# Optimization experiments

Hardware: AMD Instinct MI355X
Metric: run time of the kernel (lower is better)

## Reference

```python
import jax, jax.numpy as jnp
import numpy as np

P, K, L = 2048, 10, 3        # pairs, paths-per-pair (cap 10), max path length
E, H = 256, 512              # kg_embed_dim, node_dim
N_ENT, N_REL = 10000, 200
N_HEADS = 4


def setup_inputs() -> dict:
    key = jax.random.key(0)
    ks = jax.random.split(key, 20)
    s = 0.05  # weight scale for numerical stability
    return {
        'rel_idx': jax.random.randint(ks[0], (P, K, L), 0, N_REL, dtype=jnp.int32),
        'ent_idx': jax.random.randint(ks[1], (P, K, L), 0, N_ENT, dtype=jnp.int32),
        'path_lens': jax.random.randint(ks[2], (P, K), 0, L + 1, dtype=jnp.int32),
        'rel_table': jax.random.normal(ks[3], (N_REL, E), jnp.float32),
        'ent_table': jax.random.normal(ks[4], (N_ENT, E), jnp.float32),
        'kg_proj_w': jax.random.normal(ks[5], (H, E), jnp.float32) * s,
        'kg_proj_b': jax.random.normal(ks[6], (H,), jnp.float32) * s,
        'w_ih': jax.random.normal(ks[7], (4 * H, 2 * H), jnp.float32) * s,
        'w_hh': jax.random.normal(ks[8], (4 * H, H), jnp.float32) * s,
        'b_ih': jax.random.normal(ks[9], (4 * H,), jnp.float32) * s,
        'b_hh': jax.random.normal(ks[10], (4 * H,), jnp.float32) * s,
        'attn_in_w': jax.random.normal(ks[11], (3 * H, H), jnp.float32) * s,
        'attn_in_b': jax.random.normal(ks[12], (3 * H,), jnp.float32) * s,
        'attn_out_w': jax.random.normal(ks[13], (H, H), jnp.float32) * s,
        'attn_out_b': jax.random.normal(ks[14], (H,), jnp.float32) * s,
        'path_proj_w': jax.random.normal(ks[15], (H, H), jnp.float32) * s,
        'path_proj_b': jax.random.normal(ks[16], (H,), jnp.float32) * s,
    }


def _forward(rel_idx, ent_idx, path_lens, rel_table, ent_table, kg_proj_w, kg_proj_b,
             w_ih, w_hh, b_ih, b_hh, attn_in_w, attn_in_b, attn_out_w, attn_out_b,
             path_proj_w, path_proj_b):
    # --- encode_path, batched over all P*K paths ---
    rel_e = rel_table[rel_idx]                      # [P,K,L,E]
    ent_e = ent_table[ent_idx]                      # [P,K,L,E]
    rel_p = rel_e @ kg_proj_w.T + kg_proj_b         # [P,K,L,H]
    ent_p = ent_e @ kg_proj_w.T + kg_proj_b
    x = jnp.concatenate([rel_p, ent_p], axis=-1)    # [P,K,L,2H]
    Npk = P * K
    xs = x.reshape(Npk, L, 2 * H).transpose(1, 0, 2)  # [L,N,2H]

    h0 = jnp.zeros((Npk, H), x.dtype)
    c0 = jnp.zeros((Npk, H), x.dtype)

    def lstm_step(carry, x_t):
        h, c = carry
        g = x_t @ w_ih.T + b_ih + h @ w_hh.T + b_hh   # [N,4H], torch gate order i,f,g,o
        i, f, gg, o = jnp.split(g, 4, axis=-1)
        c = jax.nn.sigmoid(f) * c + jax.nn.sigmoid(i) * jnp.tanh(gg)
        h = jax.nn.sigmoid(o) * jnp.tanh(c)
        return (h, c), h

    _, hs = jax.lax.scan(lstm_step, (h0, c0), xs)     # [L,N,H]
    hs = hs.transpose(1, 0, 2)                        # [N,L,H]
    lens = path_lens.reshape(Npk)                     # [N]
    last = jnp.clip(lens - 1, 0, L - 1)
    h_last = jnp.take_along_axis(hs, last[:, None, None], axis=1)[:, 0]  # [N,H]
    path_emb = jnp.where(lens[:, None] > 0, h_last, 0.0).reshape(P, K, H)

    # --- per-pair multi-head self-attention over K path embeddings ---
    wq, wk, wv = jnp.split(attn_in_w, 3, axis=0)
    bq, bk, bv = jnp.split(attn_in_b, 3, axis=0)
    Dh = H // N_HEADS
    q = (path_emb @ wq.T + bq).reshape(P, K, N_HEADS, Dh)
    k = (path_emb @ wk.T + bk).reshape(P, K, N_HEADS, Dh)
    v = (path_emb @ wv.T + bv).reshape(P, K, N_HEADS, Dh)
    scores = jnp.einsum('pqhd,pkhd->phqk', q, k) / jnp.sqrt(jnp.array(Dh, x.dtype))
    attn = jax.nn.softmax(scores, axis=-1)
    ctx = jnp.einsum('phqk,pkhd->pqhd', attn, v).reshape(P, K, H)
    attn_out = ctx @ attn_out_w.T + attn_out_b        # [P,K,H]
    agg = attn_out.mean(axis=1)                       # [P,H]  (aggregated.mean(dim=1))
    return agg @ path_proj_w.T + path_proj_b          # [P,H]


def reference(rel_idx, ent_idx, path_lens, rel_table, ent_table, kg_proj_w, kg_proj_b,
              w_ih, w_hh, b_ih, b_hh, attn_in_w, attn_in_b, attn_out_w, attn_out_b,
              path_proj_w, path_proj_b):
    return _forward(rel_idx, ent_idx, path_lens, rel_table, ent_table, kg_proj_w,
                    kg_proj_b, w_ih, w_hh, b_ih, b_hh, attn_in_w, attn_in_b,
                    attn_out_w, attn_out_b, path_proj_w, path_proj_b)
```

## Files before the change

### kernel.cpp

```cpp
#include <hip/hip_runtime.h>
#include <cstdint>
#include <cstddef>

#define PP 2048
#define KK 10
#define HH 512
#define NPK (PP*KK)
#define ENT_PAD 10112
#define REL_PAD 256
#define HALF_PAIRS 1024
#define HALF_ROWS (HALF_PAIRS*KK)

using f32x4  = __attribute__((ext_vector_type(4))) float;
using short8 = __attribute__((ext_vector_type(8))) short;

__device__ __forceinline__ float sigf(float x) { return 1.0f / (1.0f + expf(-x)); }

__device__ __forceinline__ ushort f2bf(float x) {
    union { float f; uint32_t u; } v; v.f = x;
    uint32_t r = v.u + 0x7FFF + ((v.u >> 16) & 1);
    return (ushort)(r >> 16);
}
__device__ __forceinline__ float bf2f(ushort u) {
    union { uint32_t u; float f; } v; v.u = ((uint32_t)u) << 16;
    return v.f;
}

__global__ __launch_bounds__(256) void perm_bias(int* __restrict__ perm,
                                                 float* __restrict__ bihh,
                                                 const float* __restrict__ b_ih,
                                                 const float* __restrict__ b_hh) {
    int p = blockIdx.x * 256 + threadIdx.x;
    if (p < 2048) {
        int uh = p >> 6, g = (p >> 4) & 3, ul = p & 15;
        int old = g * 512 + uh * 16 + ul;
        perm[p] = old;
        bihh[p] = b_ih[old] + b_hh[old];
    }
}

__global__ __launch_bounds__(256) void transpose_k(const float* __restrict__ src,
                                                   float* __restrict__ dst, int R, int C) {
    __shared__ float t[32][33];
    int bx = blockIdx.x * 32, by = blockIdx.y * 32;
    int x = threadIdx.x & 31, y = threadIdx.x >> 5;
    for (int i = y; i < 32; i += 8) {
        int r = by + i, c = bx + x;
        if (r < R && c < C) t[i][x] = src[(size_t)r * C + c];
    }
    __syncthreads();
    for (int i = y; i < 32; i += 8) {
        int c = bx + i, r = by + x;
        if (r < R && c < C) dst[(size_t)c * R + r] = t[x][i];
    }
}

__global__ __launch_bounds__(256) void rowdot(const float* __restrict__ A, int lda,
                                              const float* __restrict__ vec, int Kd,
                                              const float* __restrict__ add1,
                                              float* __restrict__ out, int M) {
    int w = threadIdx.x >> 6, lane = threadIdx.x & 63;
    int row = blockIdx.x * 4 + w;
    if (row >= M) return;
    float acc = 0.f;
    for (int k = lane; k < Kd; k += 64) acc += A[(size_t)row * lda + k] * vec[k];
    for (int off = 32; off; off >>= 1) acc += __shfl_down(acc, off, 64);
    if (lane == 0) {
        float r = acc;
        if (add1) r += add1[row];
        out[row] = r;
    }
}

__global__ __launch_bounds__(256) void f2bf_split2d(const float* __restrict__ src,
                                                    int lda, int col0,
                                                    ushort* __restrict__ hi,
                                                    ushort* __restrict__ lo,
                                                    int nsrc_rows, int ncols, int ndst_rows,
                                                    const int* __restrict__ perm) {
    int i = blockIdx.x * 256 + threadIdx.x;
    int nc4 = ncols >> 2;
    if (i >= ndst_rows * nc4) return;
    int row = i / nc4, c4 = i % nc4;
    ushort4 h = make_ushort4(0, 0, 0, 0), l = make_ushort4(0, 0, 0, 0);
    if (row < nsrc_rows) {
        int sr = perm ? perm[row] : row;
        float4 v = *reinterpret_cast<const float4*>(src + (size_t)sr * lda + col0 + c4 * 4);
        h = make_ushort4(f2bf(v.x), f2bf(v.y), f2bf(v.z), f2bf(v.w));
        l = make_ushort4(f2bf(v.x - bf2f(h.x)), f2bf(v.y - bf2f(h.y)),
                         f2bf(v.z - bf2f(h.z)), f2bf(v.w - bf2f(h.w)));
    }
    reinterpret_cast<ushort4*>(hi)[i] = h;
    reinterpret_cast<ushort4*>(lo)[i] = l;
}

__global__ __launch_bounds__(256) void f2bf_k(const float* __restrict__ s,
                                              ushort* __restrict__ d, int n4) {
    int i = blockIdx.x * 256 + threadIdx.x;
    if (i < n4) {
        float4 v = reinterpret_cast<const float4*>(s)[i];
        reinterpret_cast<ushort4*>(d)[i] = make_ushort4(f2bf(v.x), f2bf(v.y), f2bf(v.z), f2bf(v.w));
    }
}

__global__ __launch_bounds__(256) void f2bf_perm_rows(const float* __restrict__ s,
                                                      ushort* __restrict__ d,
                                                      const int* __restrict__ perm,
                                                      int nrows, int ncols4) {
    int i = blockIdx.x * 256 + threadIdx.x;
    if (i >= nrows * ncols4) return;
    int row = i / ncols4, c4 = i % ncols4;
    int sr = perm[row];
    float4 v = reinterpret_cast<const float4*>(s + (size_t)sr * ncols4 * 4)[c4];
    reinterpret_cast<ushort4*>(d + (size_t)row * ncols4 * 4)[c4] =
        make_ushort4(f2bf(v.x), f2bf(v.y), f2bf(v.z), f2bf(v.w));
}

__global__ __launch_bounds__(256) void gemm_bf16(
    const ushort* __restrict__ A, const ushort* __restrict__ B,
    float* __restrict__ C, int M, int N, int K, int ldc,
    const float* __restrict__ bias)
{
    __shared__ ushort As[128 * 64];
    __shared__ ushort Bs[128 * 64];
    int tid = threadIdx.x;
    int lane = tid & 63;
    int w = tid >> 6;
    int wr = w >> 1, wc = w & 1;
    int col0 = blockIdx.x * 128, row0 = blockIdx.y * 128;

    f32x4 acc[4][4];
#pragma unroll
    for (int m = 0; m < 4; ++m)
#pragma unroll
        for (int n = 0; n < 4; ++n) acc[m][n] = {0.f, 0.f, 0.f, 0.f};

    int rA = lane & 15;
    int kq = lane >> 4;

    for (int kt = 0; kt < K; kt += 64) {
#pragma unroll
        for (int it = 0; it < 4; ++it) {
            int c = it * 256 + tid;
            int row = c >> 3, ch = c & 7;
            int cs = ch ^ (row & 7);
            uint4 va = *reinterpret_cast<const uint4*>(A + (size_t)(row0 + row) * K + kt + ch * 8);
            *reinterpret_cast<uint4*>(&As[(size_t)row * 64 + cs * 8]) = va;
            uint4 vb = *reinterpret_cast<const uint4*>(B + (size_t)(col0 + row) * K + kt + ch * 8);
            *reinterpret_cast<uint4*>(&Bs[(size_t)row * 64 + cs * 8]) = vb;
        }
        __syncthreads();
#pragma unroll
        for (int s = 0; s < 2; ++s) {
            int csw = (s * 4 + kq) ^ (rA & 7);
            short8 af[4], bfr[4];
#pragma unroll
            for (int m = 0; m < 4; ++m) {
                int rowA = wr * 64 + m * 16 + rA;
                af[m] = *reinterpret_cast<const short8*>(&As[(size_t)rowA * 64 + csw * 8]);
            }
#pragma unroll
            for (int n = 0; n < 4; ++n) {
                int rowB = wc * 64 + n * 16 + rA;
                bfr[n] = *reinterpret_cast<const short8*>(&Bs[(size_t)rowB * 64 + csw * 8]);
            }
#pragma unroll
            for (int m = 0; m < 4; ++m)
#pragma unroll
                for (int n = 0; n < 4; ++n)
                    acc[m][n] = __builtin_amdgcn_mfma_f32_16x16x32_bf16(af[m], bfr[n], acc[m][n], 0, 0, 0);
        }
        __syncthreads();
    }
#pragma unroll
    for (int n = 0; n < 4; ++n) {
        int gcol = col0 + wc * 64 + n * 16 + rA;
        float bv = bias ? bias[gcol] : 0.f;
#pragma unroll
        for (int m = 0; m < 4; ++m) {
            int grow0 = row0 + wr * 64 + m * 16 + kq * 4;
#pragma unroll
            for (int r = 0; r < 4; ++r)
                C[(size_t)(grow0 + r) * ldc + gcol] = acc[m][n][r] + bv;
        }
    }
}

__global__ __launch_bounds__(256) void gemm_bf16s(
    const ushort* __restrict__ Ah, const ushort* __restrict__ Al,
    const ushort* __restrict__ Bh, const ushort* __restrict__ Bl,
    float* __restrict__ C, int M, int N, int K, int ldc,
    const float* __restrict__ bias)
{
    __shared__ ushort Ash[128 * 64];
    __shared__ ushort Asl[128 * 64];
    __shared__ ushort Bsh[128 * 64];
    __shared__ ushort Bsl[128 * 64];
    int tid = threadIdx.x;
    int lane = tid & 63;
    int w = tid >> 6;
    int wr = w >> 1, wc = w & 1;
    int col0 = blockIdx.x * 128, row0 = blockIdx.y * 128;

    f32x4 acc[4][4];
#pragma unroll
    for (int m = 0; m < 4; ++m)
#pragma unroll
        for (int n = 0; n < 4; ++n) acc[m][n] = {0.f, 0.f, 0.f, 0.f};

    int rA = lane & 15;
    int kq = lane >> 4;

    for (int kt = 0; kt < K; kt += 64) {
#pragma unroll
        for (int it = 0; it < 4; ++it) {
            int c = it * 256 + tid;
            int row = c >> 3, ch = c & 7;
            int cs = ch ^ (row & 7);
            size_t ga = (size_t)(row0 + row) * K + kt + ch * 8;
            size_t gb = (size_t)(col0 + row) * K + kt + ch * 8;
            size_t la = (size_t)row * 64 + cs * 8;
            *reinterpret_cast<uint4*>(&Ash[la]) = *reinterpret_cast<const uint4*>(Ah + ga);
            *reinterpret_cast<uint4*>(&Asl[la]) = *reinterpret_cast<const uint4*>(Al + ga);
            *reinterpret_cast<uint4*>(&Bsh[la]) = *reinterpret_cast<const uint4*>(Bh + gb);
            *reinterpret_cast<uint4*>(&Bsl[la]) = *reinterpret_cast<const uint4*>(Bl + gb);
        }
        __syncthreads();
#pragma unroll
        for (int s = 0; s < 2; ++s) {
            int csw = (s * 4 + kq) ^ (rA & 7);
            short8 xh[4], yh[4], t4[4];
#pragma unroll
            for (int m = 0; m < 4; ++m) {
                int rowA = wr * 64 + m * 16 + rA;
                xh[m] = *reinterpret_cast<const short8*>(&Ash[(size_t)rowA * 64 + csw * 8]);
            }
#pragma unroll
            for (int n = 0; n < 4; ++n) {
                int rowB = wc * 64 + n * 16 + rA;
                yh[n] = *reinterpret_cast<const short8*>(&Bsh[(size_t)rowB * 64 + csw * 8]);
            }
#pragma unroll
            for (int m = 0; m < 4; ++m)
#pragma unroll
                for (int n = 0; n < 4; ++n)
                    acc[m][n] = __builtin_amdgcn_mfma_f32_16x16x32_bf16(xh[m], yh[n], acc[m][n], 0, 0, 0);
#pragma unroll
            for (int n = 0; n < 4; ++n) {
                int rowB = wc * 64 + n * 16 + rA;
                t4[n] = *reinterpret_cast<const short8*>(&Bsl[(size_t)rowB * 64 + csw * 8]);
            }
#pragma unroll
            for (int m = 0; m < 4; ++m)
#pragma unroll
                for (int n = 0; n < 4; ++n)
                    acc[m][n] = __builtin_amdgcn_mfma_f32_16x16x32_bf16(xh[m], t4[n], acc[m][n], 0, 0, 0);
#pragma unroll
            for (int m = 0; m < 4; ++m) {
                int rowA = wr * 64 + m * 16 + rA;
                t4[m] = *reinterpret_cast<const short8*>(&Asl[(size_t)rowA * 64 + csw * 8]);
            }
#pragma unroll
            for (int m = 0; m < 4; ++m)
#pragma unroll
                for (int n = 0; n < 4; ++n)
                    acc[m][n] = __builtin_amdgcn_mfma_f32_16x16x32_bf16(t4[m], yh[n], acc[m][n], 0, 0, 0);
        }
        __syncthreads();
    }
#pragma unroll
    for (int n = 0; n < 4; ++n) {
        int gcol = col0 + wc * 64 + n * 16 + rA;
        float bv = bias ? bias[gcol] : 0.f;
#pragma unroll
        for (int m = 0; m < 4; ++m) {
            int grow0 = row0 + wr * 64 + m * 16 + kq * 4;
#pragma unroll
            for (int r = 0; r < 4; ++r)
                C[(size_t)(grow0 + r) * ldc + gcol] = acc[m][n][r] + bv;
        }
    }
}

__global__ __launch_bounds__(256) void gemm_lstm(
    const ushort* __restrict__ A, const ushort* __restrict__ B,
    const float* __restrict__ relg, const float* __restrict__ entg,
    const int* __restrict__ rel_idx, const int* __restrict__ ent_idx,
    const int* __restrict__ lens_,
    ushort* __restrict__ hbuf, float* __restrict__ cbuf, ushort* __restrict__ pemb,
    int t)
{
    __shared__ ushort As[128 * 64];
    __shared__ ushort Bs[128 * 64];
    const int K = 512;
    int tid = threadIdx.x;
    int lane = tid & 63;
    int w = tid >> 6;
    int wr = w >> 1, wc = w & 1;
    int col0 = blockIdx.x * 128, row0 = blockIdx.y * 128;

    f32x4 acc[4][4];
#pragma unroll
    for (int m = 0; m < 4; ++m)
#pragma unroll
        for (int n = 0; n < 4; ++n) acc[m][n] = {0.f, 0.f, 0.f, 0.f};

    int rA = lane & 15;
    int kq = lane >> 4;

    for (int kt = 0; kt < K; kt += 64) {
#pragma unroll
        for (int it = 0; it < 4; ++it) {
            int c = it * 256 + tid;
            int row = c >> 3, ch = c & 7;
            int cs = ch ^ (row & 7);
            uint4 va = *reinterpret_cast<const uint4*>(A + (size_t)(row0 + row) * K + kt + ch * 8);
            *reinterpret_cast<uint4*>(&As[(size_t)row * 64 + cs * 8]) = va;
            uint4 vb = *reinterpret_cast<const uint4*>(B + (size_t)(col0 + row) * K + kt + ch * 8);
            *reinterpret_cast<uint4*>(&Bs[(size_t)row * 64 + cs * 8]) = vb;
        }
        __syncthreads();
#pragma unroll
        for (int s = 0; s < 2; ++s) {
            int csw = (s * 4 + kq) ^ (rA & 7);
            short8 af[4], bfr[4];
#pragma unroll
            for (int m = 0; m < 4; ++m) {
                int rowA = wr * 64 + m * 16 + rA;
                af[m] = *reinterpret_cast<const short8*>(&As[(size_t)rowA * 64 + csw * 8]);
            }
#pragma unroll
            for (int n = 0; n < 4; ++n) {
                int rowB = wc * 64 + n * 16 + rA;
                bfr[n] = *reinterpret_cast<const short8*>(&Bs[(size_t)rowB * 64 + csw * 8]);
            }
#pragma unroll
            for (int m = 0; m < 4; ++m)
#pragma unroll
                for (int n = 0; n < 4; ++n)
                    acc[m][n] = __builtin_amdgcn_mfma_f32_16x16x32_bf16(af[m], bfr[n], acc[m][n], 0, 0, 0);
        }
        __syncthreads();
    }

    int uh = blockIdx.x * 2 + wc;
    int u  = uh * 16 + rA;
    int colbase = uh * 64 + rA;
#pragma unroll
    for (int m = 0; m < 4; ++m) {
#pragma unroll
        for (int r = 0; r < 4; ++r) {
            int n = row0 + wr * 64 + m * 16 + kq * 4 + r;
            int ri = rel_idx[n * 3 + t];
            int ei = ent_idx[n * 3 + t];
            const float* rr = relg + (size_t)ri * 2048 + colbase;
            const float* er = entg + (size_t)ei * 2048 + colbase;
            float gi = acc[m][0][r] + rr[0]  + er[0];
            float gf = acc[m][1][r] + rr[16] + er[16];
            float gg = acc[m][2][r] + rr[32] + er[32];
            float go = acc[m][3][r] + rr[48] + er[48];
            float cold = cbuf[(size_t)n * 512 + u];
            float cn = sigf(gf) * cold + sigf(gi) * tanhf(gg);
            float hn = sigf(go) * tanhf(cn);
            cbuf[(size_t)n * 512 + u] = cn;
            ushort hu = f2bf(hn);
            hbuf[(size_t)n * 512 + u] = hu;
            int len = lens_[n];
            int last = len - 1;
            if (last < 0) last = 0;
            if (last > 2) last = 2;
            if (last == t) pemb[(size_t)n * 512 + u] = (len > 0) ? hu : (ushort)0;
        }
    }
}

__global__ __launch_bounds__(256) void lstm_t0(
    const float* __restrict__ relg, const float* __restrict__ entg,
    const int* __restrict__ rel_idx, const int* __restrict__ ent_idx,
    const int* __restrict__ lens_,
    ushort* __restrict__ hbuf, float* __restrict__ cbuf, ushort* __restrict__ pemb,
    int nrows)
{
    int gid = blockIdx.x * 256 + threadIdx.x;
    if (gid >= nrows * 128) return;
    int nl = gid >> 7, q = gid & 127;
    int uh = q >> 2, ul4 = q & 3;
    int ri = rel_idx[nl * 3];
    int ei = ent_idx[nl * 3];
    const float4* rg = reinterpret_cast<const float4*>(relg + (size_t)ri * 2048);
    const float4* eg = reinterpret_cast<const float4*>(entg + (size_t)ei * 2048);
    int b4 = uh * 16 + ul4;
    float4 gi = rg[b4], gf = rg[b4 + 4], gg = rg[b4 + 8], go = rg[b4 + 12];
    float4 e0 = eg[b4], e1 = eg[b4 + 4], e2 = eg[b4 + 8], e3 = eg[b4 + 12];
    gi.x += e0.x; gi.y += e0.y; gi.z += e0.z; gi.w += e0.w;
    gf.x += e1.x; gf.y += e1.y; gf.z += e1.z; gf.w += e1.w;
    gg.x += e2.x; gg.y += e2.y; gg.z += e2.z; gg.w += e2.w;
    go.x += e3.x; go.y += e3.y; go.z += e3.z; go.w += e3.w;
    (void)gf;
    float4 cn, hn;
    cn.x = sigf(gi.x) * tanhf(gg.x); hn.x = sigf(go.x) * tanhf(cn.x);
    cn.y = sigf(gi.y) * tanhf(gg.y); hn.y = sigf(go.y) * tanhf(cn.y);
    cn.z = sigf(gi.z) * tanhf(gg.z); hn.z = sigf(go.z) * tanhf(cn.z);
    cn.w = sigf(gi.w) * tanhf(gg.w); hn.w = sigf(go.w) * tanhf(cn.w);
    int u4 = uh * 4 + ul4;
    reinterpret_cast<float4*>(cbuf + (size_t)nl * 512)[u4] = cn;
    ushort4 hu = make_ushort4(f2bf(hn.x), f2bf(hn.y), f2bf(hn.z), f2bf(hn.w));
    reinterpret_cast<ushort4*>(hbuf + (size_t)nl * 512)[u4] = hu;
    int len = lens_[nl];
    int last = len - 1;
    if (last < 0) last = 0;
    if (last > 2) last = 2;
    if (last == 0) {
        ushort4 pv = (len > 0) ? hu : make_ushort4(0, 0, 0, 0);
        reinterpret_cast<ushort4*>(pemb + (size_t)nl * 512)[u4] = pv;
    }
}

__global__ __launch_bounds__(256) void attn_kernel(const float* __restrict__ qkv,
                                                   float* __restrict__ mctx, int pair0)
{
    __shared__ float qk[10][1024];
    __shared__ float sc[4][10][10];
    __shared__ float wb[4][10];
    int tid = threadIdx.x;
    const float* base = qkv + (size_t)blockIdx.x * 10 * 1536;
    for (int i = tid; i < 2560; i += 256) {
        int row = i >> 8, c4 = i & 255;
        reinterpret_cast<float4*>(&qk[row][0])[c4] =
            reinterpret_cast<const float4*>(base + (size_t)row * 1536)[c4];
    }
    __syncthreads();
    const float scale = 0.08838834764831845f;
    for (int idx = tid; idx < 400; idx += 256) {
        int h = idx / 100, rem = idx % 100, qi = rem / 10, ki = rem % 10;
        const float* qp = &qk[qi][h * 128];
        const float* kp = &qk[ki][512 + h * 128];
        float a = 0.f;
        for (int d = 0; d < 128; ++d) a += qp[d] * kp[d];
        sc[h][qi][ki] = a * scale;
    }
    __syncthreads();
    if (tid < 40) {
        int h = tid / 10, qi = tid % 10;
        float m = -1e30f;
        for (int ki = 0; ki < 10; ++ki) m = fmaxf(m, sc[h][qi][ki]);
        float ex[10]; float s = 0.f;
        for (int ki = 0; ki < 10; ++ki) { ex[ki] = expf(sc[h][qi][ki] - m); s += ex[ki]; }
        float inv = 1.f / s;
        for (int ki = 0; ki < 10; ++ki) sc[h][qi][ki] = ex[ki] * inv;
    }
    __syncthreads();
    if (tid < 40) {
        int h = tid / 10, ki = tid % 10;
        float s = 0.f;
        for (int qi = 0; qi < 10; ++qi) s += sc[h][qi][ki];
        wb[h][ki] = s * 0.1f;
    }
    __syncthreads();
    for (int e = tid; e < 512; e += 256) {
        int h = e >> 7, d = e & 127;
        float a = 0.f;
        for (int ki = 0; ki < 10; ++ki)
            a += wb[h][ki] * base[(size_t)ki * 1536 + 1024 + h * 128 + d];
        mctx[(size_t)(pair0 + blockIdx.x) * 512 + e] = a;
    }
}

extern "C" void kernel_launch(void* const* d_in, const int* in_sizes, int n_in,
                              void* d_out, int out_size, void* d_ws, size_t ws_size,
                              hipStream_t stream)
{
    const int* rel_idx     = (const int*)d_in[0];
    const int* ent_idx     = (const int*)d_in[1];
    const int* path_lens   = (const int*)d_in[2];
    const float* rel_table = (const float*)d_in[3];
    const float* ent_table = (const float*)d_in[4];
    const float* kg_proj_w = (const float*)d_in[5];
    const float* kg_proj_b = (const float*)d_in[6];
    const float* w_ih      = (const float*)d_in[7];
    const float* w_hh      = (const float*)d_in[8];
    const float* b_ih      = (const float*)d_in[9];
    const float* b_hh      = (const float*)d_in[10];
    const float* attn_in_w = (const float*)d_in[11];
    const float* attn_in_b = (const float*)d_in[12];
    const float* attn_out_w = (const float*)d_in[13];
    const float* attn_out_b = (const float*)d_in[14];
    const float* path_proj_w = (const float*)d_in[15];
    const float* path_proj_b = (const float*)d_in[16];
    float* out = (float*)d_out;
    (void)in_sizes; (void)n_in; (void)out_size; (void)ws_size;

    float* ws = (float*)d_ws;
    size_t off = 0;
    auto alloc = [&](size_t n) { float* p = ws + off; off += (n + 63) & ~(size_t)63; return p; };
    int*    perm  = (int*)alloc(2048);
    float*  bihh  = alloc(2048);
    float*  bcomb = alloc(512);
    float*  relg  = alloc((size_t)REL_PAD * 2048);
    float*  entg  = alloc((size_t)ENT_PAD * 2048);
    float*  mctx  = alloc((size_t)PP * 512);
    ushort* whhB  = (ushort*)alloc((size_t)2048 * 256);
    ushort* aiwB  = (ushort*)alloc((size_t)1536 * 256);
    ushort* pch   = (ushort*)alloc((size_t)NPK * 256);
    ushort* Wch   = (ushort*)alloc((size_t)512 * 256);
    ushort* Wcl   = (ushort*)alloc((size_t)512 * 256);
    float* R = alloc((size_t)21000000);

    size_t ro = 0;
    auto ral = [&](size_t n) { float* p = R + ro; ro += n; return p; };
    ushort* kgWh  = (ushort*)ral(65536);   ushort* kgWl  = (ushort*)ral(65536);
    ushort* relBh = (ushort*)ral(32768);   ushort* relBl = (ushort*)ral(32768);
    ushort* entBh = (ushort*)ral(1294336); ushort* entBl = (ushort*)ral(1294336);
    ushort* wrelh = (ushort*)ral(524288);  ushort* wrell = (ushort*)ral(524288);
    ushort* wenth = (ushort*)ral(524288);  ushort* wentl = (ushort*)ral(524288);
    float*  rel_pf = ral(131072);
    float*  ent_pf = ral(5177344);
    ushort* rel_ph = (ushort*)ral(65536);   ushort* rel_pl = (ushort*)ral(65536);
    ushort* ent_ph = (ushort*)ral(2588672); ushort* ent_pl = (ushort*)ral(2588672);
    float*  aoT    = ral(262144);
    ushort* pph  = (ushort*)ral(131072); ushort* ppl  = (ushort*)ral(131072);
    ushort* aoTh = (ushort*)ral(131072); ushort* aoTl = (ushort*)ral(131072);
    float*  WcombF = ral(262144);
    float*  cb = R;
    ushort* hA = (ushort*)(R + 10485760);
    ushort* hB = (ushort*)(R + 15728640);
    float*  qkv = R;
    ushort* mch = (ushort*)R;
    ushort* mcl = (ushort*)(R + 524288);

    auto split = [&](const float* src, int lda, int col0, ushort* hi, ushort* lo,
                     int nsrc, int ncols, int ndst, const int* pm) {
        int total = ndst * (ncols / 4);
        f2bf_split2d<<<(total + 255) / 256, 256, 0, stream>>>(src, lda, col0, hi, lo, nsrc, ncols, ndst, pm);
    };
    auto gemms = [&](const ushort* Ah, const ushort* Al, const ushort* Bh, const ushort* Bl,
                     float* Cp, int M, int N, int Kd, int ldc, const float* bias) {
        gemm_bf16s<<<dim3((unsigned)(N / 128), (unsigned)(M / 128)), 256, 0, stream>>>(
            Ah, Al, Bh, Bl, Cp, M, N, Kd, ldc, bias);
    };

    perm_bias<<<8, 256, 0, stream>>>(perm, bihh, b_ih, b_hh);
    transpose_k<<<dim3(16, 16), 256, 0, stream>>>(attn_out_w, aoT, 512, 512);
    split(kg_proj_w, 256, 0, kgWh, kgWl, 512, 256, 512, nullptr);
    split(rel_table, 256, 0, relBh, relBl, 200, 256, REL_PAD, nullptr);
    split(ent_table, 256, 0, entBh, entBl, 10000, 256, ENT_PAD, nullptr);
    split(w_ih, 1024, 0,   wrelh, wrell, 2048, 512, 2048, perm);
    split(w_ih, 1024, 512, wenth, wentl, 2048, 512, 2048, perm);
    split(path_proj_w, 512, 0, pph, ppl, 512, 512, 512, nullptr);
    split(aoT, 512, 0, aoTh, aoTl, 512, 512, 512, nullptr);
    f2bf_perm_rows<<<1024, 256, 0, stream>>>(w_hh, whhB, perm, 2048, 128);
    f2bf_k<<<768, 256, 0, stream>>>(attn_in_w, aiwB, 1536 * 128);
    rowdot<<<128, 256, 0, stream>>>(path_proj_w, 512, attn_out_b, 512, path_proj_b, bcomb, 512);

    gemms(relBh, relBl, kgWh, kgWl, rel_pf, REL_PAD, 512, 256, 512, kg_proj_b);
    gemms(entBh, entBl, kgWh, kgWl, ent_pf, ENT_PAD, 512, 256, 512, kg_proj_b);
    split(rel_pf, 512, 0, rel_ph, rel_pl, REL_PAD, 512, REL_PAD, nullptr);
    split(ent_pf, 512, 0, ent_ph, ent_pl, ENT_PAD, 512, ENT_PAD, nullptr);
    gemms(rel_ph, rel_pl, wrelh, wrell, relg, REL_PAD, 2048, 512, 2048, bihh);
    gemms(ent_ph, ent_pl, wenth, wentl, entg, ENT_PAD, 2048, 512, 2048, nullptr);
    gemms(pph, ppl, aoTh, aoTl, WcombF, 512, 512, 512, 512, nullptr);
    split(WcombF, 512, 0, Wch, Wcl, 512, 512, 512, nullptr);

    lstm_t0<<<(NPK * 128) / 256, 256, 0, stream>>>(
        relg, entg, rel_idx, ent_idx, path_lens, hA, cb, pch, NPK);
    gemm_lstm<<<dim3(16, 160), 256, 0, stream>>>(
        hA, whhB, relg, entg, rel_idx, ent_idx, path_lens, hB, cb, pch, 1);
    gemm_lstm<<<dim3(16, 160), 256, 0, stream>>>(
        hB, whhB, relg, entg, rel_idx, ent_idx, path_lens, hA, cb, pch, 2);

    for (int h = 0; h < 2; ++h) {
        gemm_bf16<<<dim3(12, 80), 256, 0, stream>>>(
            pch + (size_t)h * HALF_ROWS * 512, aiwB, qkv, HALF_ROWS, 1536, 512, 1536, attn_in_b);
        attn_kernel<<<HALF_PAIRS, 256, 0, stream>>>(qkv, mctx, h * HALF_PAIRS);
    }

    split(mctx, 512, 0, mch, mcl, 2048, 512, 2048, nullptr);
    gemms(mch, mcl, Wch, Wcl, out, 2048, 512, 512, 512, bcomb);
}
```

Baseline: 745.2 us.

## Fuse bf16 hi/lo splits into GEMM epilogues and interleave gate columns

The split-GEMM epilogue can now write bf16 hi/lo pairs directly, so the separate split kernels after the kg projection, the Wcomb GEMM and the attention output are removed, along with their fp32 intermediates. Gate columns of the input-gate tables are reordered so that the four gates of each unit sit next to each other, letting the LSTM kernels fetch them with one float4 load per table instead of four strided scalar loads. gemm_lstm also remaps its flattened block index with a swizzle to change L2 locality across tiles. The cost is an extra permutation array and a more complex epilogue.

```diff
diff --git a/kernel.cpp b/kernel.cpp
--- a/kernel.cpp
+++ b/kernel.cpp
@@ -26,16 +26,19 @@
     return v.f;
 }
 
-__global__ __launch_bounds__(256) void perm_bias(int* __restrict__ perm,
-                                                 float* __restrict__ bihh,
-                                                 const float* __restrict__ b_ih,
-                                                 const float* __restrict__ b_hh) {
-    int p = blockIdx.x * 256 + threadIdx.x;
-    if (p < 2048) {
-        int uh = p >> 6, g = (p >> 4) & 3, ul = p & 15;
-        int old = g * 512 + uh * 16 + ul;
-        perm[p] = old;
-        bihh[p] = b_ih[old] + b_hh[old];
+__global__ __launch_bounds__(256) void perm_bias2(int* __restrict__ perm_p,
+                                                  int* __restrict__ perm_q,
+                                                  float* __restrict__ bihh_q,
+                                                  const float* __restrict__ b_ih,
+                                                  const float* __restrict__ b_hh) {
+    int i = blockIdx.x * 256 + threadIdx.x;
+    if (i < 2048) {
+        int uh = i >> 6, g = (i >> 4) & 3, ul = i & 15;
+        perm_p[i] = g * 512 + uh * 16 + ul;
+        int u = i >> 2, gq = i & 3;
+        int oldq = gq * 512 + u;
+        perm_q[i] = oldq;
+        bihh_q[i] = b_ih[oldq] + b_hh[oldq];
     }
 }
 
@@ -189,7 +192,8 @@
 __global__ __launch_bounds__(256) void gemm_bf16s(
     const ushort* __restrict__ Ah, const ushort* __restrict__ Al,
     const ushort* __restrict__ Bh, const ushort* __restrict__ Bl,
-    float* __restrict__ C, int M, int N, int K, int ldc,
+    float* __restrict__ C, ushort* __restrict__ Chi, ushort* __restrict__ Clo,
+    int M, int N, int K, int ldc,
     const float* __restrict__ bias)
 {
     __shared__ ushort Ash[128 * 64];
@@ -276,8 +280,16 @@
         for (int m = 0; m < 4; ++m) {
             int grow0 = row0 + wr * 64 + m * 16 + kq * 4;
 #pragma unroll
-            for (int r = 0; r < 4; ++r)
-                C[(size_t)(grow0 + r) * ldc + gcol] = acc[m][n][r] + bv;
+            for (int r = 0; r < 4; ++r) {
+                float v = acc[m][n][r] + bv;
+                size_t idx = (size_t)(grow0 + r) * ldc + gcol;
+                if (C) C[idx] = v;
+                if (Chi) {
+                    ushort h = f2bf(v);
+                    Chi[idx] = h;
+                    Clo[idx] = f2bf(v - bf2f(h));
+                }
+            }
         }
     }
 }
@@ -293,11 +305,14 @@
     __shared__ ushort As[128 * 64];
     __shared__ ushort Bs[128 * 64];
     const int K = 512;
+    int L = blockIdx.x;
+    int swz = (L & 7) * 320 + (L >> 3);
+    int bx = swz & 15, by = swz >> 4;
     int tid = threadIdx.x;
     int lane = tid & 63;
     int w = tid >> 6;
     int wr = w >> 1, wc = w & 1;
-    int col0 = blockIdx.x * 128, row0 = blockIdx.y * 128;
+    int col0 = bx * 128, row0 = by * 128;
 
     f32x4 acc[4][4];
 #pragma unroll
@@ -343,9 +358,10 @@
         __syncthreads();
     }
 
-    int uh = blockIdx.x * 2 + wc;
+    int uh = bx * 2 + wc;
     int u  = uh * 16 + rA;
-    int colbase = uh * 64 + rA;
+    const float4* rel4 = reinterpret_cast<const float4*>(relg);
+    const float4* ent4 = reinterpret_cast<const float4*>(entg);
 #pragma unroll
     for (int m = 0; m < 4; ++m) {
 #pragma unroll
@@ -353,12 +369,12 @@
             int n = row0 + wr * 64 + m * 16 + kq * 4 + r;
             int ri = rel_idx[n * 3 + t];
             int ei = ent_idx[n * 3 + t];
-            const float* rr = relg + (size_t)ri * 2048 + colbase;
-            const float* er = entg + (size_t)ei * 2048 + colbase;
-            float gi = acc[m][0][r] + rr[0]  + er[0];
-            float gf = acc[m][1][r] + rr[16] + er[16];
-            float gg = acc[m][2][r] + rr[32] + er[32];
-            float go = acc[m][3][r] + rr[48] + er[48];
+            float4 rv = rel4[(size_t)ri * 512 + u];
+            float4 ev = ent4[(size_t)ei * 512 + u];
+            float gi = acc[m][0][r] + rv.x + ev.x;
+            float gf = acc[m][1][r] + rv.y + ev.y;
+            float gg = acc[m][2][r] + rv.z + ev.z;
+            float go = acc[m][3][r] + rv.w + ev.w;
             float cold = cbuf[(size_t)n * 512 + u];
             float cn = sigf(gf) * cold + sigf(gi) * tanhf(gg);
             float hn = sigf(go) * tanhf(cn);
@@ -384,40 +400,37 @@
     int gid = blockIdx.x * 256 + threadIdx.x;
     if (gid >= nrows * 128) return;
     int nl = gid >> 7, q = gid & 127;
-    int uh = q >> 2, ul4 = q & 3;
     int ri = rel_idx[nl * 3];
     int ei = ent_idx[nl * 3];
-    const float4* rg = reinterpret_cast<const float4*>(relg + (size_t)ri * 2048);
-    const float4* eg = reinterpret_cast<const float4*>(entg + (size_t)ei * 2048);
-    int b4 = uh * 16 + ul4;
-    float4 gi = rg[b4], gf = rg[b4 + 4], gg = rg[b4 + 8], go = rg[b4 + 12];
-    float4 e0 = eg[b4], e1 = eg[b4 + 4], e2 = eg[b4 + 8], e3 = eg[b4 + 12];
-    gi.x += e0.x; gi.y += e0.y; gi.z += e0.z; gi.w += e0.w;
-    gf.x += e1.x; gf.y += e1.y; gf.z += e1.z; gf.w += e1.w;
-    gg.x += e2.x; gg.y += e2.y; gg.z += e2.z; gg.w += e2.w;
-    go.x += e3.x; go.y += e3.y; go.z += e3.z; go.w += e3.w;
-    (void)gf;
+    const float4* rg = reinterpret_cast<const float4*>(relg) + (size_t)ri * 512;
+    const float4* eg = reinterpret_cast<const float4*>(entg) + (size_t)ei * 512;
     float4 cn, hn;
-    cn.x = sigf(gi.x) * tanhf(gg.x); hn.x = sigf(go.x) * tanhf(cn.x);
-    cn.y = sigf(gi.y) * tanhf(gg.y); hn.y = sigf(go.y) * tanhf(cn.y);
-    cn.z = sigf(gi.z) * tanhf(gg.z); hn.z = sigf(go.z) * tanhf(cn.z);
-    cn.w = sigf(gi.w) * tanhf(gg.w); hn.w = sigf(go.w) * tanhf(cn.w);
-    int u4 = uh * 4 + ul4;
-    reinterpret_cast<float4*>(cbuf + (size_t)nl * 512)[u4] = cn;
+#pragma unroll
+    for (int j = 0; j < 4; ++j) {
+        float4 a = rg[q * 4 + j];
+        float4 b = eg[q * 4 + j];
+        float gi = a.x + b.x, gg = a.z + b.z, go = a.w + b.w;
+        float c = sigf(gi) * tanhf(gg);
+        float h = sigf(go) * tanhf(c);
+        (&cn.x)[j] = c;
+        (&hn.x)[j] = h;
+    }
+    reinterpret_cast<float4*>(cbuf + (size_t)nl * 512)[q] = cn;
     ushort4 hu = make_ushort4(f2bf(hn.x), f2bf(hn.y), f2bf(hn.z), f2bf(hn.w));
-    reinterpret_cast<ushort4*>(hbuf + (size_t)nl * 512)[u4] = hu;
+    reinterpret_cast<ushort4*>(hbuf + (size_t)nl * 512)[q] = hu;
     int len = lens_[nl];
     int last = len - 1;
     if (last < 0) last = 0;
     if (last > 2) last = 2;
     if (last == 0) {
         ushort4 pv = (len > 0) ? hu : make_ushort4(0, 0, 0, 0);
-        reinterpret_cast<ushort4*>(pemb + (size_t)nl * 512)[u4] = pv;
+        reinterpret_cast<ushort4*>(pemb + (size_t)nl * 512)[q] = pv;
     }
 }
 
 __global__ __launch_bounds__(256) void attn_kernel(const float* __restrict__ qkv,
-                                                   float* __restrict__ mctx, int pair0)
+                                                   ushort* __restrict__ mch,
+                                                   ushort* __restrict__ mcl, int pair0)
 {
     __shared__ float qk[10][1024];
     __shared__ float sc[4][10][10];
@@ -462,7 +475,10 @@
         float a = 0.f;
         for (int ki = 0; ki < 10; ++ki)
             a += wb[h][ki] * base[(size_t)ki * 1536 + 1024 + h * 128 + d];
-        mctx[(size_t)(pair0 + blockIdx.x) * 512 + e] = a;
+        size_t idx = (size_t)(pair0 + blockIdx.x) * 512 + e;
+        ushort hh = f2bf(a);
+        mch[idx] = hh;
+        mcl[idx] = f2bf(a - bf2f(hh));
     }
 }
 
@@ -493,17 +509,19 @@
     float* ws = (float*)d_ws;
     size_t off = 0;
     auto alloc = [&](size_t n) { float* p = ws + off; off += (n + 63) & ~(size_t)63; return p; };
-    int*    perm  = (int*)alloc(2048);
-    float*  bihh  = alloc(2048);
-    float*  bcomb = alloc(512);
-    float*  relg  = alloc((size_t)REL_PAD * 2048);
-    float*  entg  = alloc((size_t)ENT_PAD * 2048);
-    float*  mctx  = alloc((size_t)PP * 512);
-    ushort* whhB  = (ushort*)alloc((size_t)2048 * 256);
-    ushort* aiwB  = (ushort*)alloc((size_t)1536 * 256);
-    ushort* pch   = (ushort*)alloc((size_t)NPK * 256);
-    ushort* Wch   = (ushort*)alloc((size_t)512 * 256);
-    ushort* Wcl   = (ushort*)alloc((size_t)512 * 256);
+    int*    perm_p = (int*)alloc(2048);
+    int*    perm_q = (int*)alloc(2048);
+    float*  bihh   = alloc(2048);
+    float*  bcomb  = alloc(512);
+    float*  relg   = alloc((size_t)REL_PAD * 2048);
+    float*  entg   = alloc((size_t)ENT_PAD * 2048);
+    ushort* whhB   = (ushort*)alloc((size_t)2048 * 256);
+    ushort* aiwB   = (ushort*)alloc((size_t)1536 * 256);
+    ushort* pch    = (ushort*)alloc((size_t)NPK * 256);
+    ushort* Wch    = (ushort*)alloc((size_t)512 * 256);
+    ushort* Wcl    = (ushort*)alloc((size_t)512 * 256);
+    ushort* mch    = (ushort*)alloc((size_t)PP * 256);
+    ushort* mcl    = (ushort*)alloc((size_t)PP * 256);
     float* R = alloc((size_t)21000000);
 
     size_t ro = 0;
@@ -513,20 +531,15 @@
     ushort* entBh = (ushort*)ral(1294336); ushort* entBl = (ushort*)ral(1294336);
     ushort* wrelh = (ushort*)ral(524288);  ushort* wrell = (ushort*)ral(524288);
     ushort* wenth = (ushort*)ral(524288);  ushort* wentl = (ushort*)ral(524288);
-    float*  rel_pf = ral(131072);
-    float*  ent_pf = ral(5177344);
     ushort* rel_ph = (ushort*)ral(65536);   ushort* rel_pl = (ushort*)ral(65536);
     ushort* ent_ph = (ushort*)ral(2588672); ushort* ent_pl = (ushort*)ral(2588672);
     float*  aoT    = ral(262144);
     ushort* pph  = (ushort*)ral(131072); ushort* ppl  = (ushort*)ral(131072);
     ushort* aoTh = (ushort*)ral(131072); ushort* aoTl = (ushort*)ral(131072);
-    float*  WcombF = ral(262144);
     float*  cb = R;
     ushort* hA = (ushort*)(R + 10485760);
     ushort* hB = (ushort*)(R + 15728640);
     float*  qkv = R;
-    ushort* mch = (ushort*)R;
-    ushort* mcl = (ushort*)(R + 524288);
 
     auto split = [&](const float* src, int lda, int col0, ushort* hi, ushort* lo,
                      int nsrc, int ncols, int ndst, const int* pm) {
@@ -534,46 +547,43 @@
         f2bf_split2d<<<(total + 255) / 256, 256, 0, stream>>>(src, lda, col0, hi, lo, nsrc, ncols, ndst, pm);
     };
     auto gemms = [&](const ushort* Ah, const ushort* Al, const ushort* Bh, const ushort* Bl,
-                     float* Cp, int M, int N, int Kd, int ldc, const float* bias) {
+                     float* Cp, ushort* Chi, ushort* Clo,
+                     int M, int N, int Kd, int ldc, const float* bias) {
         gemm_bf16s<<<dim3((unsigned)(N / 128), (unsigned)(M / 128)), 256, 0, stream>>>(
-            Ah, Al, Bh, Bl, Cp, M, N, Kd, ldc, bias);
+            Ah, Al, Bh, Bl, Cp, Chi, Clo, M, N, Kd, ldc, bias);
     };
 
-    perm_bias<<<8, 256, 0, stream>>>(perm, bihh, b_ih, b_hh);
+    perm_bias2<<<8, 256, 0, stream>>>(perm_p, perm_q, bihh, b_ih, b_hh);
     transpose_k<<<dim3(16, 16), 256, 0, stream>>>(attn_out_w, aoT, 512, 512);
     split(kg_proj_w, 256, 0, kgWh, kgWl, 512, 256, 512, nullptr);
     split(rel_table, 256, 0, relBh, relBl, 200, 256, REL_PAD, nullptr);
     split(ent_table, 256, 0, entBh, entBl, 10000, 256, ENT_PAD, nullptr);
-    split(w_ih, 1024, 0,   wrelh, wrell, 2048, 512, 2048, perm);
-    split(w_ih, 1024, 512, wenth, wentl, 2048, 512, 2048, perm);
+    split(w_ih, 1024, 0,   wrelh, wrell, 2048, 512, 2048, perm_q);
+    split(w_ih, 1024, 512, wenth, wentl, 2048, 512, 2048, perm_q);
     split(path_proj_w, 512, 0, pph, ppl, 512, 512, 512, nullptr);
     split(aoT, 512, 0, aoTh, aoTl, 512, 512, 512, nullptr);
-    f2bf_perm_rows<<<1024, 256, 0, stream>>>(w_hh, whhB, perm, 2048, 128);
+    f2bf_perm_rows<<<1024, 256, 0, stream>>>(w_hh, whhB, perm_p, 2048, 128);
     f2bf_k<<<768, 256, 0, stream>>>(attn_in_w, aiwB, 1536 * 128);
     rowdot<<<128, 256, 0, stream>>>(path_proj_w, 512, attn_out_b, 512, path_proj_b, bcomb, 512);
 
-    gemms(relBh, relBl, kgWh, kgWl, rel_pf, REL_PAD, 512, 256, 512, kg_proj_b);
-    gemms(entBh, entBl, kgWh, kgWl, ent_pf, ENT_PAD, 512, 256, 512, kg_proj_b);
-    split(rel_pf, 512, 0, rel_ph, rel_pl, REL_PAD, 512, REL_PAD, nullptr);
-    split(ent_pf, 512, 0, ent_ph, ent_pl, ENT_PAD, 512, ENT_PAD, nullptr);
-    gemms(rel_ph, rel_pl, wrelh, wrell, relg, REL_PAD, 2048, 512, 2048, bihh);
-    gemms(ent_ph, ent_pl, wenth, wentl, entg, ENT_PAD, 2048, 512, 2048, nullptr);
-    gemms(pph, ppl, aoTh, aoTl, WcombF, 512, 512, 512, 512, nullptr);
-    split(WcombF, 512, 0, Wch, Wcl, 512, 512, 512, nullptr);
+    gemms(relBh, relBl, kgWh, kgWl, nullptr, rel_ph, rel_pl, REL_PAD, 512, 256, 512, kg_proj_b);
+    gemms(entBh, entBl, kgWh, kgWl, nullptr, ent_ph, ent_pl, ENT_PAD, 512, 256, 512, kg_proj_b);
+    gemms(rel_ph, rel_pl, wrelh, wrell, relg, nullptr, nullptr, REL_PAD, 2048, 512, 2048, bihh);
+    gemms(ent_ph, ent_pl, wenth, wentl, entg, nullptr, nullptr, ENT_PAD, 2048, 512, 2048, nullptr);
+    gemms(pph, ppl, aoTh, aoTl, nullptr, Wch, Wcl, 512, 512, 512, 512, nullptr);
 
     lstm_t0<<<(NPK * 128) / 256, 256, 0, stream>>>(
         relg, entg, rel_idx, ent_idx, path_lens, hA, cb, pch, NPK);
-    gemm_lstm<<<dim3(16, 160), 256, 0, stream>>>(
+    gemm_lstm<<<2560, 256, 0, stream>>>(
         hA, whhB, relg, entg, rel_idx, ent_idx, path_lens, hB, cb, pch, 1);
-    gemm_lstm<<<dim3(16, 160), 256, 0, stream>>>(
+    gemm_lstm<<<2560, 256, 0, stream>>>(
         hB, whhB, relg, entg, rel_idx, ent_idx, path_lens, hA, cb, pch, 2);
 
     for (int h = 0; h < 2; ++h) {
         gemm_bf16<<<dim3(12, 80), 256, 0, stream>>>(
             pch + (size_t)h * HALF_ROWS * 512, aiwB, qkv, HALF_ROWS, 1536, 512, 1536, attn_in_b);
-        attn_kernel<<<HALF_PAIRS, 256, 0, stream>>>(qkv, mctx, h * HALF_PAIRS);
-    }
-
-    split(mctx, 512, 0, mch, mcl, 2048, 512, 2048, nullptr);
-    gemms(mch, mcl, Wch, Wcl, out, 2048, 512, 512, 512, bcomb);
-}
+        attn_kernel<<<HALF_PAIRS, 256, 0, stream>>>(qkv, mch, mcl, h * HALF_PAIRS);
+    }
+
+    gemms(mch, mcl, Wch, Wcl, out, nullptr, nullptr, 2048, 512, 512, 512, bcomb);
+}
```

Result: slower. 768.4 us (+3.1%).
